# Optimization experiments

Measured on AMD Instinct MI355X. Metric: run time of the kernel, lower is better.

## Reference

```python
import jax, jax.numpy as jnp
import numpy as np

D_MODEL = 1024
HEADS = 16
HEAD_DIM = D_MODEL // HEADS


def setup_inputs() -> dict:
    key = jax.random.key(0)
    ks = jax.random.split(key, 9)
    s = 1.0 / np.sqrt(D_MODEL)
    inp = {
        "inputs": jax.random.normal(ks[0], (4, 2048, D_MODEL), dtype=jnp.float32),
        "Wq": jax.random.normal(ks[1], (D_MODEL, D_MODEL), dtype=jnp.float32) * s,
        "bq": jnp.zeros((D_MODEL,), dtype=jnp.float32),
        "Wk": jax.random.normal(ks[2], (D_MODEL, D_MODEL), dtype=jnp.float32) * s,
        "bk": jnp.zeros((D_MODEL,), dtype=jnp.float32),
        "Wv": jax.random.normal(ks[3], (D_MODEL, D_MODEL), dtype=jnp.float32) * s,
        "bv": jnp.zeros((D_MODEL,), dtype=jnp.float32),
        "Wo": jax.random.normal(ks[4], (D_MODEL, D_MODEL), dtype=jnp.float32) * s,
        "bo": jnp.zeros((D_MODEL,), dtype=jnp.float32),
    }
    return inp


def reference(inputs, Wq, bq, Wk, bk, Wv, bv, Wo, bo):
    bs, seq, _ = inputs.shape
    # projections -> [b, h, s, d]
    def split_heads(x):
        return x.reshape(bs, seq, HEADS, HEAD_DIM).transpose(0, 2, 1, 3)
    q = split_heads(inputs @ Wq + bq)
    k = split_heads(inputs @ Wk + bk)
    v = split_heads(inputs @ Wv + bv)
    # NOTE: original code divides by (head_dim ** 1 / 2) == head_dim/2, not sqrt(head_dim)
    scale = HEAD_DIM / 2.0
    scores = jnp.einsum("bhqd,bhkd->bhqk", q, k) / scale
    attn = jax.nn.softmax(scores, axis=-1)
    out = jnp.einsum("bhqk,bhkd->bhqd", attn, v)
    out = out.transpose(0, 2, 1, 3).reshape(bs, seq, HEADS * HEAD_DIM)
    return out @ Wo + bo
```

## Files before the change

kernel.cpp:

```cpp
#include <hip/hip_runtime.h>
#include <stdint.h>

typedef __attribute__((ext_vector_type(8))) short bf16x8;
typedef __attribute__((ext_vector_type(4))) float f32x4;
typedef __attribute__((address_space(1))) void as1_void;
typedef __attribute__((address_space(3))) void as3_void;

#define D_MODEL 1024
#define SEQ     2048
#define BATCH   4
#define HEADS   16
#define HDIM    64

#define QSCALE 0.045084220029218407f

__device__ __forceinline__ ushort f2bf(float f) {
  union { float f; unsigned u; } v; v.f = f;
  unsigned u = v.u + 0x7fffu + ((v.u >> 16) & 1u);
  return (ushort)(u >> 16);
}

__device__ __forceinline__ void gload_lds16(const void* g, void* l) {
  __builtin_amdgcn_global_load_lds((as1_void*)(uintptr_t)g, (as3_void*)l, 16, 0, 0);
}

__device__ __forceinline__ bf16x8 pack8(float a0, float a1, float a2, float a3,
                                        float a4, float a5, float a6, float a7) {
  union { uint u[4]; bf16x8 v; } x;
  x.u[0] = __builtin_amdgcn_perm(__float_as_uint(a1), __float_as_uint(a0), 0x07060302);
  x.u[1] = __builtin_amdgcn_perm(__float_as_uint(a3), __float_as_uint(a2), 0x07060302);
  x.u[2] = __builtin_amdgcn_perm(__float_as_uint(a5), __float_as_uint(a4), 0x07060302);
  x.u[3] = __builtin_amdgcn_perm(__float_as_uint(a7), __float_as_uint(a6), 0x07060302);
  return x.v;
}

__global__ void prep_kernel(const float* __restrict__ X,
                            const float* w0, const float* w1, const float* w2, const float* w3,
                            const float* __restrict__ bq, const float* __restrict__ bk,
                            const float* __restrict__ bv,
                            ushort* __restrict__ Xb, ushort* __restrict__ WT,
                            float* __restrict__ bcat) {
  __shared__ float tile[32][33];
  const int bx = blockIdx.x, t = threadIdx.x;
  if (bx < 8192) {
    int i = bx * 256 + t;
    float4 f = reinterpret_cast<const float4*>(X)[i];
    ushort4 o;
    o.x = f2bf(f.x); o.y = f2bf(f.y); o.z = f2bf(f.z); o.w = f2bf(f.w);
    reinterpret_cast<ushort4*>(Xb)[i] = o;
  } else if (bx < 12288) {
    int tz = bx - 8192;
    int z = tz >> 10;
    int xy = tz & 1023;
    int bxt = xy & 31, byt = xy >> 5;
    const float* w = (z == 0) ? w0 : (z == 1) ? w1 : (z == 2) ? w2 : w3;
    const float sc = (z == 0) ? QSCALE : 1.0f;
    ushort* o = WT + (size_t)z * D_MODEL * D_MODEL;
    int tx = t & 31, ty = t >> 5;
    int x = bxt * 32 + tx;
    int y0 = byt * 32;
    #pragma unroll
    for (int i = ty; i < 32; i += 8)
      tile[i][tx] = w[(size_t)(y0 + i) * D_MODEL + x];
    __syncthreads();
    #pragma unroll
    for (int i = ty; i < 32; i += 8)
      o[(size_t)(bxt * 32 + i) * D_MODEL + y0 + tx] = f2bf(tile[tx][i] * sc);
  } else {
    int i = (bx - 12288) * 256 + t;
    bcat[i] = (i < 1024) ? bq[i] * QSCALE : (i < 2048) ? bk[i - 1024] : bv[i - 2048];
  }
}

#define MFMA16(a, b, c) __builtin_amdgcn_mfma_f32_16x16x32_bf16(a, b, c, 0, 0, 0)

__global__ __launch_bounds__(512, 2) void gemm_qkv(const ushort* __restrict__ A, const ushort* __restrict__ BT,
                                                   const float* __restrict__ bias,
                                                   ushort* __restrict__ QK, ushort* __restrict__ Vt) {
  __shared__ __align__(16) char smem[131072];
  const int tid  = threadIdx.x;
  const int w    = tid >> 6;
  const int lane = tid & 63;
  const int lo   = lane & 15, quad = lane >> 4;
  const int wr   = w >> 2, wc = w & 3;

  const int orig = blockIdx.y * 12 + blockIdx.x;
  const int wg   = (orig & 7) * 48 + (orig >> 3);
  const int m0   = (wg / 12) * 256;
  const int n0   = (wg % 12) * 256;

  const int tl = tid ^ ((tid >> 3) & 7);
  const ushort* sA = A  + (size_t)(m0 + (tl >> 3)) * 1024 + (tl & 7) * 8;
  const ushort* sB = BT + (size_t)(n0 + (tl >> 3)) * 1024 + (tl & 7) * 8;
  char* lw = smem + w * 1024;

  const int o0 = (quad * 16) ^ ((lo & 7) << 4);
  const int o1 = o0 ^ 64;
  const int rdA = wr * 16384 + lo * 128;
  const int rdB = 65536 + (wc * 64 + lo) * 128;

  f32x4 acc[8][4];
  #pragma unroll
  for (int i = 0; i < 8; ++i)
    #pragma unroll
    for (int j = 0; j < 4; ++j) acc[i][j] = {0.f, 0.f, 0.f, 0.f};

  gload_lds16(sB,              lw + 65536);
  gload_lds16(sB +  64 * 1024, lw + 65536 +  8192);
  gload_lds16(sB + 128 * 1024, lw + 65536 + 16384);
  gload_lds16(sB + 192 * 1024, lw + 65536 + 24576);
  gload_lds16(sA,              lw);
  gload_lds16(sA + 128 * 1024, lw + 16384);
  gload_lds16(sA +  64 * 1024, lw +  8192);
  gload_lds16(sA + 192 * 1024, lw + 24576);
  asm volatile("s_waitcnt vmcnt(2)" ::: "memory");
  __builtin_amdgcn_s_barrier();
  asm volatile("" ::: "memory");

  const char* L = smem;
  #pragma unroll 2
  for (int kt = 0; kt < 16; ++kt) {
    const int b32 = (kt & 1) << 15;
    const int nb  = b32 ^ 32768;
    const int kc  = (kt + 1) * 64;
    const bool pf = kt < 15;
    bf16x8 bfr[4][2], af0[2], af1[2];

    #pragma unroll
    for (int ni = 0; ni < 4; ++ni) {
      bfr[ni][0] = *(const bf16x8*)(L + b32 + rdB + ni * 2048 + o0);
      bfr[ni][1] = *(const bf16x8*)(L + b32 + rdB + ni * 2048 + o1);
    }
    af0[0] = *(const bf16x8*)(L + b32 + rdA + o0);
    af0[1] = *(const bf16x8*)(L + b32 + rdA + o1);
    af1[0] = *(const bf16x8*)(L + b32 + rdA + 2048 + o0);
    af1[1] = *(const bf16x8*)(L + b32 + rdA + 2048 + o1);
    if (pf) {
      gload_lds16(sB + kc,             lw + nb + 65536);
      gload_lds16(sB + 64 * 1024 + kc, lw + nb + 65536 + 8192);
    }
    asm volatile("s_waitcnt lgkmcnt(8)" ::: "memory");
    __builtin_amdgcn_s_barrier();
    asm volatile("s_waitcnt lgkmcnt(0)" ::: "memory");
    __builtin_amdgcn_sched_barrier(0);
    __builtin_amdgcn_s_setprio(1);
    #pragma unroll
    for (int ks = 0; ks < 2; ++ks)
      #pragma unroll
      for (int ni = 0; ni < 4; ++ni) {
        acc[0][ni] = MFMA16(af0[ks], bfr[ni][ks], acc[0][ni]);
        acc[1][ni] = MFMA16(af1[ks], bfr[ni][ks], acc[1][ni]);
      }
    __builtin_amdgcn_s_setprio(0);
    __builtin_amdgcn_s_barrier();
    asm volatile("" ::: "memory");

    af0[0] = *(const bf16x8*)(L + b32 + rdA + 2 * 2048 + o0);
    af0[1] = *(const bf16x8*)(L + b32 + rdA + 2 * 2048 + o1);
    af1[0] = *(const bf16x8*)(L + b32 + rdA + 3 * 2048 + o0);
    af1[1] = *(const bf16x8*)(L + b32 + rdA + 3 * 2048 + o1);
    if (pf) {
      gload_lds16(sB + 128 * 1024 + kc, lw + nb + 65536 + 16384);
      gload_lds16(sB + 192 * 1024 + kc, lw + nb + 65536 + 24576);
    }
    __builtin_amdgcn_s_barrier();
    asm volatile("s_waitcnt lgkmcnt(0)" ::: "memory");
    __builtin_amdgcn_sched_barrier(0);
    __builtin_amdgcn_s_setprio(1);
    #pragma unroll
    for (int ks = 0; ks < 2; ++ks)
      #pragma unroll
      for (int ni = 0; ni < 4; ++ni) {
        acc[2][ni] = MFMA16(af0[ks], bfr[ni][ks], acc[2][ni]);
        acc[3][ni] = MFMA16(af1[ks], bfr[ni][ks], acc[3][ni]);
      }
    __builtin_amdgcn_s_setprio(0);
    if (pf) asm volatile("s_waitcnt vmcnt(4)" ::: "memory");
    else    asm volatile("s_waitcnt vmcnt(0)" ::: "memory");
    __builtin_amdgcn_s_barrier();
    asm volatile("" ::: "memory");

    af0[0] = *(const bf16x8*)(L + b32 + rdA + 4 * 2048 + o0);
    af0[1] = *(const bf16x8*)(L + b32 + rdA + 4 * 2048 + o1);
    af1[0] = *(const bf16x8*)(L + b32 + rdA + 5 * 2048 + o0);
    af1[1] = *(const bf16x8*)(L + b32 + rdA + 5 * 2048 + o1);
    if (pf) {
      gload_lds16(sA + kc,              lw + nb);
      gload_lds16(sA + 128 * 1024 + kc, lw + nb + 16384);
    }
    __builtin_amdgcn_s_barrier();
    asm volatile("s_waitcnt lgkmcnt(0)" ::: "memory");
    __builtin_amdgcn_sched_barrier(0);
    __builtin_amdgcn_s_setprio(1);
    #pragma unroll
    for (int ks = 0; ks < 2; ++ks)
      #pragma unroll
      for (int ni = 0; ni < 4; ++ni) {
        acc[4][ni] = MFMA16(af0[ks], bfr[ni][ks], acc[4][ni]);
        acc[5][ni] = MFMA16(af1[ks], bfr[ni][ks], acc[5][ni]);
      }
    __builtin_amdgcn_s_setprio(0);
    __builtin_amdgcn_s_barrier();
    asm volatile("" ::: "memory");

    af0[0] = *(const bf16x8*)(L + b32 + rdA + 6 * 2048 + o0);
    af0[1] = *(const bf16x8*)(L + b32 + rdA + 6 * 2048 + o1);
    af1[0] = *(const bf16x8*)(L + b32 + rdA + 7 * 2048 + o0);
    af1[1] = *(const bf16x8*)(L + b32 + rdA + 7 * 2048 + o1);
    if (pf) {
      gload_lds16(sA + 64 * 1024 + kc,  lw + nb + 8192);
      gload_lds16(sA + 192 * 1024 + kc, lw + nb + 24576);
    }
    __builtin_amdgcn_s_barrier();
    asm volatile("s_waitcnt lgkmcnt(0)" ::: "memory");
    __builtin_amdgcn_sched_barrier(0);
    __builtin_amdgcn_s_setprio(1);
    #pragma unroll
    for (int ks = 0; ks < 2; ++ks)
      #pragma unroll
      for (int ni = 0; ni < 4; ++ni) {
        acc[6][ni] = MFMA16(af0[ks], bfr[ni][ks], acc[6][ni]);
        acc[7][ni] = MFMA16(af1[ks], bfr[ni][ks], acc[7][ni]);
      }
    __builtin_amdgcn_s_setprio(0);
    if (pf) asm volatile("s_waitcnt vmcnt(2)" ::: "memory");
    __builtin_amdgcn_s_barrier();
    asm volatile("" ::: "memory");
  }

  if (n0 < 2048) {
    #pragma unroll
    for (int ni = 0; ni < 4; ++ni) {
      const int col = n0 + wc * 64 + ni * 16 + lo;
      const float bv = bias[col];
      #pragma unroll
      for (int mi = 0; mi < 8; ++mi) {
        const int row = m0 + wr * 128 + mi * 16 + quad * 4;
        #pragma unroll
        for (int r = 0; r < 4; ++r)
          QK[(size_t)(row + r) * 2048 + col] = f2bf(acc[mi][ni][r] + bv);
      }
    }
  } else {
    #pragma unroll
    for (int ni = 0; ni < 4; ++ni) {
      const int col  = n0 + wc * 64 + ni * 16 + lo;
      const int vcol = col - 2048;
      const int hh = vcol >> 6, d = vcol & 63;
      const float bv = bias[col];
      #pragma unroll
      for (int mi = 0; mi < 8; ++mi) {
        const int base = m0 + wr * 128 + mi * 16;
        const int brow = base + quad * 4;
        const int bidx = brow >> 11;
        const int srow = brow & 2047;
        const int ck   = srow >> 6;
        const int c0   = (base & 32) + (quad << 3) + ((base >> 2) & 4);
        ushort e0 = f2bf(acc[mi][ni][0] + bv);
        ushort e1 = f2bf(acc[mi][ni][1] + bv);
        ushort e2 = f2bf(acc[mi][ni][2] + bv);
        ushort e3 = f2bf(acc[mi][ni][3] + bv);
        uint2 pk;
        pk.x = (uint)e0 | ((uint)e1 << 16);
        pk.y = (uint)e2 | ((uint)e3 << 16);
        *(uint2*)&Vt[(size_t)((bidx * HEADS + hh) * HDIM + d) * SEQ + ck * 64 + c0] = pk;
      }
    }
  }
}

__global__ __launch_bounds__(256) void gemm_bt_f32(const ushort* __restrict__ A, const ushort* __restrict__ BT,
                                                   const float* __restrict__ bias, float* __restrict__ C,
                                                   int M, int N, int K) {
  __shared__ __align__(16) ushort As[128 * 32];
  __shared__ __align__(16) ushort Bs[128 * 32];
  const int tid  = threadIdx.x;
  const int w    = tid >> 6;
  const int lane = tid & 63;
  const int lo   = lane & 15, quad = lane >> 4;
  const int m0 = blockIdx.y * 128, n0 = blockIdx.x * 128;
  const int ra = lane >> 2;
  const int ca = (lane & 3) * 8;
  const int wm = (w & 1) * 64, wn = (w >> 1) * 64;

  f32x4 acc[4][4];
  #pragma unroll
  for (int i = 0; i < 4; ++i)
    #pragma unroll
    for (int j = 0; j < 4; ++j) acc[i][j] = {0.f, 0.f, 0.f, 0.f};

  for (int k0 = 0; k0 < K; k0 += 32) {
    #pragma unroll
    for (int i = 0; i < 2; ++i) {
      const int j = w * 2 + i;
      gload_lds16(A  + (size_t)(m0 + j * 16 + ra) * K + k0 + ca, &As[j * 512]);
      gload_lds16(BT + (size_t)(n0 + j * 16 + ra) * K + k0 + ca, &Bs[j * 512]);
    }
    __syncthreads();
    bf16x8 af[4], bfv[4];
    #pragma unroll
    for (int mi = 0; mi < 4; ++mi) af[mi]  = *(const bf16x8*)&As[(wm + mi * 16 + lo) * 32 + quad * 8];
    #pragma unroll
    for (int ni = 0; ni < 4; ++ni) bfv[ni] = *(const bf16x8*)&Bs[(wn + ni * 16 + lo) * 32 + quad * 8];
    #pragma unroll
    for (int mi = 0; mi < 4; ++mi)
      #pragma unroll
      for (int ni = 0; ni < 4; ++ni)
        acc[mi][ni] = __builtin_amdgcn_mfma_f32_16x16x32_bf16(af[mi], bfv[ni], acc[mi][ni], 0, 0, 0);
    __syncthreads();
  }

  #pragma unroll
  for (int ni = 0; ni < 4; ++ni) {
    const int col = n0 + wn + ni * 16 + lo;
    const float bv = bias[col];
    #pragma unroll
    for (int mi = 0; mi < 4; ++mi) {
      #pragma unroll
      for (int r = 0; r < 4; ++r) {
        const int row = m0 + wm + mi * 16 + quad * 4 + r;
        C[(size_t)row * N + col] = acc[mi][ni][r] + bv;
      }
    }
  }
}

__global__ __launch_bounds__(256, 2) void attn_kernel(const ushort* __restrict__ QK,
                                                      const ushort* __restrict__ Vt,
                                                      ushort* __restrict__ Og) {
  __shared__ __align__(16) ushort Ks[64 * 64];
  __shared__ __align__(16) ushort Vs[64 * 64];

  const int tid  = threadIdx.x;
  const int w    = tid >> 6, lane = tid & 63;
  const int lo   = lane & 15, quad = lane >> 4;
  const int h = blockIdx.y, b = blockIdx.z;
  const int qbase = blockIdx.x * 256 + w * 64;
  const int swz = lo & 7;

  bf16x8 qf[4][2];
  #pragma unroll
  for (int qg = 0; qg < 4; ++qg) {
    const ushort* qp = QK + (size_t)(b * SEQ + qbase + qg * 16 + lo) * 2048 + h * HDIM;
    qf[qg][0] = *(const bf16x8*)(qp + quad * 8);
    qf[qg][1] = *(const bf16x8*)(qp + 32 + quad * 8);
  }

  f32x4 acc[4][4];
  #pragma unroll
  for (int qg = 0; qg < 4; ++qg)
    #pragma unroll
    for (int t = 0; t < 4; ++t) acc[qg][t] = {0.f, 0.f, 0.f, 0.f};
  float lsum[4] = {0.f, 0.f, 0.f, 0.f};

  for (int ck = 0; ck < SEQ / 64; ++ck) {
    __syncthreads();
    #pragma unroll
    for (int i = 0; i < 2; ++i) {
      const int c16 = (w * 2 + i) * 64 + lane;
      const int r = c16 >> 3, ps = c16 & 7;
      const int gs = ps ^ (r & 7);
      gload_lds16(QK + (size_t)(b * SEQ + ck * 64 + r) * 2048 + 1024 + h * HDIM + gs * 8,
                  &Ks[(w * 2 + i) * 512]);
      gload_lds16(Vt + (size_t)((b * HEADS + h) * HDIM + r) * SEQ + ck * 64 + gs * 8,
                  &Vs[(w * 2 + i) * 512]);
    }
    __syncthreads();

    bf16x8 kf[4][2];
    #pragma unroll
    for (int sub = 0; sub < 4; ++sub) {
      const ushort* kr = &Ks[(sub * 16 + lo) * 64];
      kf[sub][0] = *(const bf16x8*)(kr + ((quad ^ swz) * 8));
      kf[sub][1] = *(const bf16x8*)(kr + (((4 + quad) ^ swz) * 8));
    }

    bf16x8 af[4][2];
    #pragma unroll
    for (int qg = 0; qg < 4; ++qg) {
      f32x4 s[4];
      #pragma unroll
      for (int sub = 0; sub < 4; ++sub) s[sub] = {0.f, 0.f, 0.f, 0.f};
      #pragma unroll
      for (int sub = 0; sub < 4; ++sub) {
        s[sub] = __builtin_amdgcn_mfma_f32_16x16x32_bf16(kf[sub][0], qf[qg][0], s[sub], 0, 0, 0);
        s[sub] = __builtin_amdgcn_mfma_f32_16x16x32_bf16(kf[sub][1], qf[qg][1], s[sub], 0, 0, 0);
      }
      float p[4][4];
      #pragma unroll
      for (int sub = 0; sub < 4; ++sub)
        #pragma unroll
        for (int r = 0; r < 4; ++r) p[sub][r] = __builtin_amdgcn_exp2f(s[sub][r]);
      float t0 = 0.f;
      #pragma unroll
      for (int sub = 0; sub < 4; ++sub)
        t0 += (p[sub][0] + p[sub][1]) + (p[sub][2] + p[sub][3]);
      lsum[qg] += t0;
      af[qg][0] = pack8(p[0][0], p[0][1], p[0][2], p[0][3], p[1][0], p[1][1], p[1][2], p[1][3]);
      af[qg][1] = pack8(p[2][0], p[2][1], p[2][2], p[2][3], p[3][0], p[3][1], p[3][2], p[3][3]);
    }

    #pragma unroll
    for (int t = 0; t < 4; ++t) {
      const ushort* vr = &Vs[(t * 16 + lo) * 64];
      #pragma unroll
      for (int hh = 0; hh < 2; ++hh) {
        bf16x8 vf = *(const bf16x8*)(vr + (((hh * 4 + quad) ^ swz) * 8));
        #pragma unroll
        for (int qg = 0; qg < 4; ++qg)
          acc[qg][t] = __builtin_amdgcn_mfma_f32_16x16x32_bf16(af[qg][hh], vf, acc[qg][t], 0, 0, 0);
      }
    }
  }

  #pragma unroll
  for (int qg = 0; qg < 4; ++qg) {
    float v = lsum[qg];
    v += __shfl_xor(v, 16);
    v += __shfl_xor(v, 32);
    float linv[4];
    #pragma unroll
    for (int r = 0; r < 4; ++r) linv[r] = 1.0f / __shfl(v, quad * 4 + r);
    #pragma unroll
    for (int t = 0; t < 4; ++t)
      #pragma unroll
      for (int r = 0; r < 4; ++r)
        Og[(size_t)(b * SEQ + qbase + qg * 16 + quad * 4 + r) * D_MODEL + h * HDIM + t * 16 + lo] =
            f2bf(acc[qg][t][r] * linv[r]);
  }
}

extern "C" void kernel_launch(void* const* d_in, const int* in_sizes, int n_in,
                              void* d_out, int out_size, void* d_ws, size_t ws_size,
                              hipStream_t stream) {
  const float* X  = (const float*)d_in[0];
  const float* Wq = (const float*)d_in[1];
  const float* bq = (const float*)d_in[2];
  const float* Wk = (const float*)d_in[3];
  const float* bk = (const float*)d_in[4];
  const float* Wv = (const float*)d_in[5];
  const float* bv = (const float*)d_in[6];
  const float* Wo = (const float*)d_in[7];
  const float* bo = (const float*)d_in[8];
  float* out = (float*)d_out;
  char* ws = (char*)d_ws;

  ushort* Xb  = (ushort*)(ws);
  ushort* WT  = (ushort*)(ws + 16777216);
  ushort* QKb = (ushort*)(ws + 25165824);
  ushort* Vtb = (ushort*)(ws + 58720256);
  ushort* Ob  = (ushort*)(ws + 75497472);
  float*  bcat = (float*)(ws + 75497472);
  const int WSTRIDE = D_MODEL * D_MODEL;

  prep_kernel<<<12300, 256, 0, stream>>>(X, Wq, Wk, Wv, Wo, bq, bk, bv, Xb, WT, bcat);

  gemm_qkv<<<dim3(12, 32), 512, 0, stream>>>(Xb, WT, bcat, QKb, Vtb);

  attn_kernel<<<dim3(SEQ / 256, HEADS, BATCH), 256, 0, stream>>>(QKb, Vtb, Ob);

  gemm_bt_f32<<<dim3(8, 64), 256, 0, stream>>>(Ob, WT + 3 * WSTRIDE, bo, out,
                                               BATCH * SEQ, D_MODEL, D_MODEL);
}
```

Measured before the change: 260.5 us.

## Double-buffer K/V tiles in attention with async prefetch and block remap

The attention kernel now stages K and V into two LDS buffers and issues the global-to-LDS loads for the next chunk before computing on the current one. It waits on the older loads with an explicit vmcnt count and raw barriers instead of __syncthreads. Block indices are remapped so that neighbouring blocks share a head and batch, which should improve L2 reuse of K/V. Wave priority is raised around the PV MFMA section. LDS use doubles, which may affect occupancy, and the hand-written vmcnt count depends on the compiler not adding other outstanding loads.

```diff
diff --git a/kernel.cpp b/kernel.cpp
--- a/kernel.cpp
+++ b/kernel.cpp
@@ -328,49 +328,66 @@
 __global__ __launch_bounds__(256, 2) void attn_kernel(const ushort* __restrict__ QK,
                                                       const ushort* __restrict__ Vt,
                                                       ushort* __restrict__ Og) {
-  __shared__ __align__(16) ushort Ks[64 * 64];
-  __shared__ __align__(16) ushort Vs[64 * 64];
+  __shared__ __align__(16) ushort Ks[2][64 * 64];
+  __shared__ __align__(16) ushort Vs[2][64 * 64];
 
   const int tid  = threadIdx.x;
   const int w    = tid >> 6, lane = tid & 63;
   const int lo   = lane & 15, quad = lane >> 4;
-  const int h = blockIdx.y, b = blockIdx.z;
-  const int qbase = blockIdx.x * 256 + w * 64;
+
+  const int p  = blockIdx.x + (blockIdx.y << 3) + (blockIdx.z << 7);
+  const int G  = ((p >> 6) << 3) | (p & 7);
+  const int h  = G & 15, b = G >> 4;
+  const int qbase = ((p >> 3) & 7) * 256 + w * 64;
   const int swz = lo & 7;
 
-  bf16x8 qf[4][2];
-  #pragma unroll
-  for (int qg = 0; qg < 4; ++qg) {
-    const ushort* qp = QK + (size_t)(b * SEQ + qbase + qg * 16 + lo) * 2048 + h * HDIM;
-    qf[qg][0] = *(const bf16x8*)(qp + quad * 8);
-    qf[qg][1] = *(const bf16x8*)(qp + 32 + quad * 8);
-  }
-
-  f32x4 acc[4][4];
-  #pragma unroll
-  for (int qg = 0; qg < 4; ++qg)
-    #pragma unroll
-    for (int t = 0; t < 4; ++t) acc[qg][t] = {0.f, 0.f, 0.f, 0.f};
-  float lsum[4] = {0.f, 0.f, 0.f, 0.f};
-
-  for (int ck = 0; ck < SEQ / 64; ++ck) {
-    __syncthreads();
+  auto STAGE = [&](int buf, int ck) {
     #pragma unroll
     for (int i = 0; i < 2; ++i) {
       const int c16 = (w * 2 + i) * 64 + lane;
       const int r = c16 >> 3, ps = c16 & 7;
       const int gs = ps ^ (r & 7);
       gload_lds16(QK + (size_t)(b * SEQ + ck * 64 + r) * 2048 + 1024 + h * HDIM + gs * 8,
-                  &Ks[(w * 2 + i) * 512]);
+                  &Ks[buf][(w * 2 + i) * 512]);
       gload_lds16(Vt + (size_t)((b * HEADS + h) * HDIM + r) * SEQ + ck * 64 + gs * 8,
-                  &Vs[(w * 2 + i) * 512]);
-    }
-    __syncthreads();
+                  &Vs[buf][(w * 2 + i) * 512]);
+    }
+  };
+
+  bf16x8 qf[4][2];
+  #pragma unroll
+  for (int qg = 0; qg < 4; ++qg) {
+    const ushort* qp = QK + (size_t)(b * SEQ + qbase + qg * 16 + lo) * 2048 + h * HDIM;
+    qf[qg][0] = *(const bf16x8*)(qp + quad * 8);
+    qf[qg][1] = *(const bf16x8*)(qp + 32 + quad * 8);
+  }
+
+  f32x4 acc[4][4];
+  #pragma unroll
+  for (int qg = 0; qg < 4; ++qg)
+    #pragma unroll
+    for (int t = 0; t < 4; ++t) acc[qg][t] = {0.f, 0.f, 0.f, 0.f};
+  float lsum[4] = {0.f, 0.f, 0.f, 0.f};
+
+  STAGE(0, 0);
+  __syncthreads();
+
+  #pragma unroll 2
+  for (int ck = 0; ck < SEQ / 64; ++ck) {
+    const int cur = ck & 1;
+    if (ck < SEQ / 64 - 1) {
+      STAGE(cur ^ 1, ck + 1);
+      asm volatile("s_waitcnt vmcnt(4)" ::: "memory");
+    } else {
+      asm volatile("s_waitcnt vmcnt(0)" ::: "memory");
+    }
+    __builtin_amdgcn_s_barrier();
+    asm volatile("" ::: "memory");
 
     bf16x8 kf[4][2];
     #pragma unroll
     for (int sub = 0; sub < 4; ++sub) {
-      const ushort* kr = &Ks[(sub * 16 + lo) * 64];
+      const ushort* kr = &Ks[cur][(sub * 16 + lo) * 64];
       kf[sub][0] = *(const bf16x8*)(kr + ((quad ^ swz) * 8));
       kf[sub][1] = *(const bf16x8*)(kr + (((4 + quad) ^ swz) * 8));
     }
@@ -386,23 +403,24 @@
         s[sub] = __builtin_amdgcn_mfma_f32_16x16x32_bf16(kf[sub][0], qf[qg][0], s[sub], 0, 0, 0);
         s[sub] = __builtin_amdgcn_mfma_f32_16x16x32_bf16(kf[sub][1], qf[qg][1], s[sub], 0, 0, 0);
       }
-      float p[4][4];
+      float p2[4][4];
       #pragma unroll
       for (int sub = 0; sub < 4; ++sub)
         #pragma unroll
-        for (int r = 0; r < 4; ++r) p[sub][r] = __builtin_amdgcn_exp2f(s[sub][r]);
+        for (int r = 0; r < 4; ++r) p2[sub][r] = __builtin_amdgcn_exp2f(s[sub][r]);
       float t0 = 0.f;
       #pragma unroll
       for (int sub = 0; sub < 4; ++sub)
-        t0 += (p[sub][0] + p[sub][1]) + (p[sub][2] + p[sub][3]);
+        t0 += (p2[sub][0] + p2[sub][1]) + (p2[sub][2] + p2[sub][3]);
       lsum[qg] += t0;
-      af[qg][0] = pack8(p[0][0], p[0][1], p[0][2], p[0][3], p[1][0], p[1][1], p[1][2], p[1][3]);
-      af[qg][1] = pack8(p[2][0], p[2][1], p[2][2], p[2][3], p[3][0], p[3][1], p[3][2], p[3][3]);
-    }
-
+      af[qg][0] = pack8(p2[0][0], p2[0][1], p2[0][2], p2[0][3], p2[1][0], p2[1][1], p2[1][2], p2[1][3]);
+      af[qg][1] = pack8(p2[2][0], p2[2][1], p2[2][2], p2[2][3], p2[3][0], p2[3][1], p2[3][2], p2[3][3]);
+    }
+
+    __builtin_amdgcn_s_setprio(1);
     #pragma unroll
     for (int t = 0; t < 4; ++t) {
-      const ushort* vr = &Vs[(t * 16 + lo) * 64];
+      const ushort* vr = &Vs[cur][(t * 16 + lo) * 64];
       #pragma unroll
       for (int hh = 0; hh < 2; ++hh) {
         bf16x8 vf = *(const bf16x8*)(vr + (((hh * 4 + quad) ^ swz) * 8));
@@ -411,6 +429,11 @@
           acc[qg][t] = __builtin_amdgcn_mfma_f32_16x16x32_bf16(af[qg][hh], vf, acc[qg][t], 0, 0, 0);
       }
     }
+    __builtin_amdgcn_s_setprio(0);
+
+    asm volatile("" ::: "memory");
+    __builtin_amdgcn_s_barrier();
+    asm volatile("" ::: "memory");
   }
 
   #pragma unroll
```

After: 260.6 us. Within noise of the previous version (+0.0%).
